# Kernel tuning notes

Measured on AMD Instinct MI355X. Metric: run time of the kernel, lower is better.

Reference implementation:

```python
import jax, jax.numpy as jnp
import numpy as np

N_NODES = 50000
IN_CH = 128
HID = 128
OUT_CH = 64
N_EDGES = 800000


def _glorot(key, shape):
    fan_in, fan_out = shape[1], shape[0]
    lim = (6.0 / (fan_in + fan_out)) ** 0.5
    return jax.random.uniform(key, shape, jnp.float32, -lim, lim)


def setup_inputs() -> dict:
    key = jax.random.key(0)
    ks = jax.random.split(key, 10)
    x = jax.random.normal(ks[0], (N_NODES, IN_CH), jnp.float32)
    edge_index = jax.random.randint(ks[1], (2, N_EDGES), 0, N_NODES, jnp.int64)
    return {
        "x": x,
        "edge_index": edge_index,
        # SAGEConv 1: in -> hidden (lin_l has bias, lin_r no bias)
        "Wl1": _glorot(ks[2], (HID, IN_CH)),
        "bl1": jnp.zeros((HID,), jnp.float32),
        "Wr1": _glorot(ks[3], (HID, IN_CH)),
        # SAGEConv 2: hidden -> hidden
        "Wl2": _glorot(ks[4], (HID, HID)),
        "bl2": jnp.zeros((HID,), jnp.float32),
        "Wr2": _glorot(ks[5], (HID, HID)),
        # final Linear hidden -> out
        "Wout": _glorot(ks[6], (OUT_CH, HID)),
        "bout": jnp.zeros((OUT_CH,), jnp.float32),
    }


def _sage_conv(x, src, dst, Wl, bl, Wr, n_nodes):
    # mean-aggregate neighbor features: scatter x[src] into dst buckets
    msg = x[src]                                              # [E, C]
    agg = jax.ops.segment_sum(msg, dst, num_segments=n_nodes)  # [N, C]
    cnt = jax.ops.segment_sum(jnp.ones((src.shape[0],), x.dtype), dst,
                              num_segments=n_nodes)            # [N]
    agg = agg / jnp.maximum(cnt, 1.0)[:, None]
    return agg @ Wl.T + bl + x @ Wr.T


def reference(x, edge_index, Wl1, bl1, Wr1, Wl2, bl2, Wr2, Wout, bout):
    src, dst = edge_index[0], edge_index[1]
    n = x.shape[0]
    h = _sage_conv(x, src, dst, Wl1, bl1, Wr1, n)
    h = jax.nn.relu(h)
    h = _sage_conv(h, src, dst, Wl2, bl2, Wr2, n)
    logits = h @ Wout.T + bout
    return jax.nn.log_softmax(logits, axis=1)
```

## Files before the change

### kernel.cpp

```cpp
#include <hip/hip_runtime.h>

#define N_NODES 50000
#define N_EDGES 800000
#define HID 128
#define OUT_CH 64
#define LDA 264
#define BSHIFT 6
#define NBUCKET ((N_NODES + 63) >> BSHIFT)
#define NCHUNK 256
#define CHUNK_E (N_EDGES / NCHUNK)
#define BCAP 2560

typedef __attribute__((ext_vector_type(8))) short bf16x8;
typedef __attribute__((ext_vector_type(4))) float f32x4;

__device__ __forceinline__ float bf2f(unsigned int bits16) {
    return __uint_as_float(bits16 << 16);
}
__device__ __forceinline__ unsigned short f2bf(float f) {
    unsigned int u = __float_as_uint(f);
    u = (u + 0x7fffu + ((u >> 16) & 1u)) >> 16;
    return (unsigned short)u;
}
__device__ __forceinline__ void acc_u4(float* a, uint4 v) {
    a[0] += bf2f(v.x & 0xffffu); a[1] += bf2f(v.x >> 16);
    a[2] += bf2f(v.y & 0xffffu); a[3] += bf2f(v.y >> 16);
    a[4] += bf2f(v.z & 0xffffu); a[5] += bf2f(v.z >> 16);
    a[6] += bf2f(v.w & 0xffffu); a[7] += bf2f(v.w >> 16);
}

__global__ __launch_bounds__(256) void convert_x_kernel(
    const float* __restrict__ x, unsigned short* __restrict__ xb)
{
    int gid = blockIdx.x * 256 + threadIdx.x;
    int node = gid >> 5, c4 = gid & 31;
    float4 v = reinterpret_cast<const float4*>(x + (size_t)node * HID)[c4];
    unsigned short* o = xb + (size_t)node * HID + c4 * 4;
    o[0] = f2bf(v.x); o[1] = f2bf(v.y); o[2] = f2bf(v.z); o[3] = f2bf(v.w);
}

__global__ __launch_bounds__(256) void swizzle_w_kernel(
    const float* __restrict__ Wl1, const float* __restrict__ Wr1,
    const float* __restrict__ Wl2, const float* __restrict__ Wr2,
    const float* __restrict__ Wout,
    unsigned short* __restrict__ w1s, unsigned short* __restrict__ w2s,
    unsigned short* __restrict__ wos)
{
    int fid = blockIdx.x * 256 + threadIdx.x;
    if (fid < 8192) {
        int layer = fid >> 12;
        int r = fid & 4095;
        int lane = r & 63, ks = (r >> 6) & 7, t = r >> 9;
        int col = t * 16 + (lane & 15);
        int kb = ks * 32 + (lane >> 4) * 8;
        const float* Wl = layer ? Wl2 : Wl1;
        const float* Wr = layer ? Wr2 : Wr1;
        unsigned short* o = (layer ? w2s : w1s) + (size_t)r * 8;
        #pragma unroll
        for (int j = 0; j < 8; ++j) {
            int k = kb + j;
            float v = (k < 128) ? Wl[(size_t)col * 128 + k] : Wr[(size_t)col * 128 + (k - 128)];
            o[j] = f2bf(v);
        }
    } else if (fid < 9216) {
        int r = fid - 8192;
        int lane = r & 63, ks = (r >> 6) & 3, t = r >> 8;
        int col = t * 16 + (lane & 15);
        int kb = ks * 32 + (lane >> 4) * 8;
        unsigned short* o = wos + (size_t)r * 8;
        #pragma unroll
        for (int j = 0; j < 8; ++j)
            o[j] = f2bf(Wout[(size_t)col * 128 + kb + j]);
    }
}

__global__ __launch_bounds__(256) void histb_kernel(const int* __restrict__ dst,
                                                    int* __restrict__ histg) {
    __shared__ int h[NBUCKET];
    for (int i = threadIdx.x; i < NBUCKET; i += 256) h[i] = 0;
    __syncthreads();
    const int e0 = blockIdx.x * CHUNK_E;
    for (int i = threadIdx.x; i < CHUNK_E; i += 256)
        atomicAdd(&h[dst[e0 + i] >> BSHIFT], 1);
    __syncthreads();
    for (int i = threadIdx.x; i < NBUCKET; i += 256)
        histg[i * NCHUNK + blockIdx.x] = h[i];
}

__global__ __launch_bounds__(256) void scanA2_kernel(const int* __restrict__ histg,
                                                     int* __restrict__ partial) {
    const int tid = threadIdx.x;
    int v = histg[blockIdx.x * 256 + tid];
    const int lane = tid & 63, wave = tid >> 6;
    int incl = v;
    #pragma unroll
    for (int off = 1; off < 64; off <<= 1) {
        int t = __shfl_up(incl, off);
        if (lane >= off) incl += t;
    }
    __shared__ int wsum[4];
    if (lane == 63) wsum[wave] = incl;
    __syncthreads();
    if (tid == 0) partial[blockIdx.x] = wsum[0] + wsum[1] + wsum[2] + wsum[3];
}

__global__ __launch_bounds__(256) void scanB2_kernel(int* __restrict__ partial) {
    const int tid = threadIdx.x;
    int vals[4]; int sum = 0;
    #pragma unroll
    for (int j = 0; j < 4; ++j) {
        int idx = tid * 4 + j;
        vals[j] = (idx < NBUCKET) ? partial[idx] : 0;
        sum += vals[j];
    }
    const int lane = tid & 63, wave = tid >> 6;
    int incl = sum;
    #pragma unroll
    for (int off = 1; off < 64; off <<= 1) {
        int t = __shfl_up(incl, off);
        if (lane >= off) incl += t;
    }
    __shared__ int wsum[4];
    if (lane == 63) wsum[wave] = incl;
    __syncthreads();
    int base = 0;
    if (wave > 0) base += wsum[0];
    if (wave > 1) base += wsum[1];
    if (wave > 2) base += wsum[2];
    int run = base + incl - sum;
    #pragma unroll
    for (int j = 0; j < 4; ++j) {
        int idx = tid * 4 + j;
        if (idx < NBUCKET) { int c = vals[j]; partial[idx] = run; run += c; }
    }
}

__global__ __launch_bounds__(256) void scanC2_kernel(int* __restrict__ histg,
                                                     const int* __restrict__ partial) {
    const int tid = threadIdx.x;
    const int i = blockIdx.x * 256 + tid;
    int v = histg[i];
    const int lane = tid & 63, wave = tid >> 6;
    int incl = v;
    #pragma unroll
    for (int off = 1; off < 64; off <<= 1) {
        int t = __shfl_up(incl, off);
        if (lane >= off) incl += t;
    }
    __shared__ int wsum[4];
    if (lane == 63) wsum[wave] = incl;
    __syncthreads();
    int base = partial[blockIdx.x];
    if (wave > 0) base += wsum[0];
    if (wave > 1) base += wsum[1];
    if (wave > 2) base += wsum[2];
    histg[i] = base + incl - v;
}

__global__ __launch_bounds__(256) void binA_kernel(
    const int* __restrict__ src, const int* __restrict__ dst,
    const int* __restrict__ obase, unsigned* __restrict__ epack)
{
    __shared__ int cur[NBUCKET];
    for (int i = threadIdx.x; i < NBUCKET; i += 256)
        cur[i] = obase[i * NCHUNK + blockIdx.x];
    __syncthreads();
    const int e0 = blockIdx.x * CHUNK_E;
    for (int i = threadIdx.x; i < CHUNK_E; i += 256) {
        int d = dst[e0 + i];
        int p = atomicAdd(&cur[d >> BSHIFT], 1);
        epack[p] = (unsigned)src[e0 + i] | ((unsigned)(d & 63) << 16);
    }
}

__global__ __launch_bounds__(256) void bucket_sort_kernel(
    const unsigned* __restrict__ epack, const int* __restrict__ obase,
    int* __restrict__ row_ptr, unsigned short* __restrict__ esrc)
{
    __shared__ unsigned lpack[BCAP];
    __shared__ unsigned short lout[BCAP];
    __shared__ int deg[64], cur[64];
    const int b = blockIdx.x;
    const int tid = threadIdx.x;
    const int regBeg = obase[b * NCHUNK];
    const int regEnd = (b + 1 < NBUCKET) ? obase[(b + 1) * NCHUNK] : N_EDGES;
    const int cnt = regEnd - regBeg;

    if (tid < 64) deg[tid] = 0;
    __syncthreads();
    for (int i = tid; i < cnt; i += 256) {
        unsigned p = epack[regBeg + i];
        if (i < BCAP) lpack[i] = p;
        atomicAdd(&deg[(p >> 16) & 63], 1);
    }
    __syncthreads();
    if (tid < 64) {
        int v = deg[tid];
        int incl = v;
        #pragma unroll
        for (int off = 1; off < 64; off <<= 1) {
            int t = __shfl_up(incl, off);
            if (tid >= off) incl += t;
        }
        int pre = incl - v;
        cur[tid] = pre;
        int node = b * 64 + tid;
        if (node < N_NODES) row_ptr[node] = regBeg + pre;
    }
    if (b == NBUCKET - 1 && tid == 0) row_ptr[N_NODES] = N_EDGES;
    __syncthreads();
    for (int i = tid; i < cnt; i += 256) {
        unsigned p = (i < BCAP) ? lpack[i] : epack[regBeg + i];
        int q = atomicAdd(&cur[(p >> 16) & 63], 1);
        unsigned short s = (unsigned short)(p & 0xffffu);
        if (q < BCAP) lout[q] = s;
        else esrc[regBeg + q] = s;
    }
    __syncthreads();
    const int lim = (cnt < BCAP) ? cnt : BCAP;
    for (int i = tid; i < lim; i += 256)
        esrc[regBeg + i] = lout[i];
}

__global__ __launch_bounds__(256) void gather_kernel(
    const unsigned short* __restrict__ feat,
    const int* __restrict__ row_ptr, const unsigned short* __restrict__ esrc,
    unsigned short* __restrict__ agg)
{
    const int tid = threadIdx.x;
    const int wave = tid >> 6, lane = tid & 63;
    const int g = lane >> 4, c = lane & 15;
    const int gw0 = blockIdx.x * 4 + wave;
    const int NW = gridDim.x * 4;
    const int NGROUP = N_NODES / 4;

    for (int grp = gw0; grp < NGROUP; grp += NW) {
        const int base = grp * 4;
        int beg[4], deg[4], ids[4];
        int rp0 = row_ptr[base];
        #pragma unroll
        for (int j = 0; j < 4; ++j) {
            int rp1 = row_ptr[base + j + 1];
            beg[j] = rp0; deg[j] = rp1 - rp0; rp0 = rp1;
        }
        #pragma unroll
        for (int j = 0; j < 4; ++j) {
            int idx = beg[j] + c;
            idx = (idx < N_EDGES) ? idx : (N_EDGES - 1);
            ids[j] = esrc[idx];
        }

        float acc[4][8];
        #pragma unroll
        for (int j = 0; j < 4; ++j)
            #pragma unroll
            for (int k = 0; k < 8; ++k) acc[j][k] = 0.0f;

        #pragma unroll
        for (int jp = 0; jp < 2; ++jp) {
            uint4 v[2][4];
            #pragma unroll
            for (int jj = 0; jj < 2; ++jj) {
                const int j = jp * 2 + jj;
                #pragma unroll
                for (int b = 0; b < 4; ++b) {
                    int s = __shfl(ids[j], b * 4 + g);
                    v[jj][b] = *reinterpret_cast<const uint4*>(feat + (size_t)s * HID + c * 8);
                }
            }
            #pragma unroll
            for (int jj = 0; jj < 2; ++jj) {
                const int j = jp * 2 + jj;
                #pragma unroll
                for (int b = 0; b < 4; ++b) {
                    uint4 vv = v[jj][b];
                    if (b * 4 + g >= deg[j]) vv = make_uint4(0u, 0u, 0u, 0u);
                    acc_u4(acc[j], vv);
                }
            }
            #pragma unroll
            for (int jj = 0; jj < 2; ++jj) {
                const int j = jp * 2 + jj;
                const int last = beg[j] + deg[j] - 1;
                for (int e0 = 16; e0 < deg[j]; e0 += 16) {
                    int idx = beg[j] + e0 + c;
                    int id2 = esrc[(idx < last) ? idx : last];
                    uint4 w[4];
                    #pragma unroll
                    for (int b = 0; b < 4; ++b) {
                        int s = __shfl(id2, b * 4 + g);
                        w[b] = *reinterpret_cast<const uint4*>(feat + (size_t)s * HID + c * 8);
                    }
                    #pragma unroll
                    for (int b = 0; b < 4; ++b) {
                        uint4 vv = w[b];
                        if (e0 + b * 4 + g >= deg[j]) vv = make_uint4(0u, 0u, 0u, 0u);
                        acc_u4(acc[j], vv);
                    }
                }
            }
        }

        #pragma unroll
        for (int j = 0; j < 4; ++j) {
            const float scale = 1.0f / fmaxf((float)deg[j], 1.0f);
            float r[8];
            #pragma unroll
            for (int k = 0; k < 8; ++k) {
                float t = acc[j][k];
                t += __shfl_xor(t, 16);
                t += __shfl_xor(t, 32);
                r[k] = t * scale;
            }
            if (g == 0) {
                uint4 pk;
                pk.x = (unsigned)f2bf(r[0]) | ((unsigned)f2bf(r[1]) << 16);
                pk.y = (unsigned)f2bf(r[2]) | ((unsigned)f2bf(r[3]) << 16);
                pk.z = (unsigned)f2bf(r[4]) | ((unsigned)f2bf(r[5]) << 16);
                pk.w = (unsigned)f2bf(r[6]) | ((unsigned)f2bf(r[7]) << 16);
                *reinterpret_cast<uint4*>(agg + (size_t)(base + j) * HID + c * 8) = pk;
            }
        }
    }
}

__global__ __launch_bounds__(256) void sage_gemm_kernel(
    const unsigned short* __restrict__ aggIn,
    const unsigned short* __restrict__ selfIn,
    const unsigned short* __restrict__ wsz,
    const float* __restrict__ bias,
    unsigned short* __restrict__ Hout, int relu)
{
    __shared__ unsigned short sA[16 * LDA];
    const int tid = threadIdx.x;
    const int wave = tid >> 6, lane = tid & 63;
    const int m0 = blockIdx.x * 16;

    {
        int r = tid >> 4, cc = tid & 15;
        *reinterpret_cast<uint4*>(&sA[r * LDA + cc * 8]) =
            reinterpret_cast<const uint4*>(aggIn + (size_t)(m0 + r) * HID)[cc];
        *reinterpret_cast<uint4*>(&sA[r * LDA + 128 + cc * 8]) =
            reinterpret_cast<const uint4*>(selfIn + (size_t)(m0 + r) * HID)[cc];
    }
    __syncthreads();

    const int l15 = lane & 15, lq = lane >> 4;
    bf16x8 bfrag[2][8];
    #pragma unroll
    for (int nt = 0; nt < 2; ++nt) {
        const unsigned short* wb = wsz + ((size_t)(wave * 2 + nt) * 8) * 64 * 8 + lane * 8;
        #pragma unroll
        for (int ks = 0; ks < 8; ++ks)
            bfrag[nt][ks] = *reinterpret_cast<const bf16x8*>(wb + (size_t)ks * 64 * 8);
    }
    f32x4 acc0 = {0.f, 0.f, 0.f, 0.f}, acc1 = {0.f, 0.f, 0.f, 0.f};
    #pragma unroll
    for (int ks = 0; ks < 8; ++ks) {
        bf16x8 af = *reinterpret_cast<const bf16x8*>(&sA[l15 * LDA + ks * 32 + lq * 8]);
        acc0 = __builtin_amdgcn_mfma_f32_16x16x32_bf16(af, bfrag[0][ks], acc0, 0, 0, 0);
        acc1 = __builtin_amdgcn_mfma_f32_16x16x32_bf16(af, bfrag[1][ks], acc1, 0, 0, 0);
    }
    const int n0 = wave * 32;
    #pragma unroll
    for (int nt = 0; nt < 2; ++nt) {
        const f32x4 a = nt ? acc1 : acc0;
        const int col = n0 + nt * 16 + l15;
        const float bv = bias[col];
        #pragma unroll
        for (int r = 0; r < 4; ++r) {
            float v = a[r] + bv;
            if (relu) v = fmaxf(v, 0.0f);
            Hout[(size_t)(m0 + lq * 4 + r) * HID + col] = f2bf(v);
        }
    }
}

__global__ __launch_bounds__(256) void final_gemm_kernel(
    const unsigned short* __restrict__ aggIn,
    const unsigned short* __restrict__ selfIn,
    const unsigned short* __restrict__ wsz2,
    const float* __restrict__ bl2,
    const unsigned short* __restrict__ wos,
    const float* __restrict__ bout,
    float* __restrict__ out)
{
    __shared__ unsigned short sA[16 * LDA];
    __shared__ float sL[16][OUT_CH];
    const int tid = threadIdx.x;
    const int wave = tid >> 6, lane = tid & 63;
    const int m0 = blockIdx.x * 16;

    {
        int r = tid >> 4, cc = tid & 15;
        *reinterpret_cast<uint4*>(&sA[r * LDA + cc * 8]) =
            reinterpret_cast<const uint4*>(aggIn + (size_t)(m0 + r) * HID)[cc];
        *reinterpret_cast<uint4*>(&sA[r * LDA + 128 + cc * 8]) =
            reinterpret_cast<const uint4*>(selfIn + (size_t)(m0 + r) * HID)[cc];
    }
    __syncthreads();

    const int l15 = lane & 15, lq = lane >> 4;
    bf16x8 bfrag[2][8];
    #pragma unroll
    for (int nt = 0; nt < 2; ++nt) {
        const unsigned short* wb = wsz2 + ((size_t)(wave * 2 + nt) * 8) * 64 * 8 + lane * 8;
        #pragma unroll
        for (int ks = 0; ks < 8; ++ks)
            bfrag[nt][ks] = *reinterpret_cast<const bf16x8*>(wb + (size_t)ks * 64 * 8);
    }
    f32x4 acc0 = {0.f, 0.f, 0.f, 0.f}, acc1 = {0.f, 0.f, 0.f, 0.f};
    #pragma unroll
    for (int ks = 0; ks < 8; ++ks) {
        bf16x8 af = *reinterpret_cast<const bf16x8*>(&sA[l15 * LDA + ks * 32 + lq * 8]);
        acc0 = __builtin_amdgcn_mfma_f32_16x16x32_bf16(af, bfrag[0][ks], acc0, 0, 0, 0);
        acc1 = __builtin_amdgcn_mfma_f32_16x16x32_bf16(af, bfrag[1][ks], acc1, 0, 0, 0);
    }
    __syncthreads();

    const int n0 = wave * 32;
    #pragma unroll
    for (int nt = 0; nt < 2; ++nt) {
        const f32x4 a = nt ? acc1 : acc0;
        const int col = n0 + nt * 16 + l15;
        const float bv = bl2[col];
        #pragma unroll
        for (int r = 0; r < 4; ++r)
            sA[(lq * 4 + r) * LDA + col] = f2bf(a[r] + bv);
    }
    __syncthreads();

    {
        f32x4 hacc = {0.f, 0.f, 0.f, 0.f};
        #pragma unroll
        for (int ks = 0; ks < 4; ++ks) {
            bf16x8 af = *reinterpret_cast<const bf16x8*>(&sA[l15 * LDA + ks * 32 + lq * 8]);
            bf16x8 bf = *reinterpret_cast<const bf16x8*>(
                wos + ((size_t)(wave * 4 + ks)) * 64 * 8 + lane * 8);
            hacc = __builtin_amdgcn_mfma_f32_16x16x32_bf16(af, bf, hacc, 0, 0, 0);
        }
        const int col = wave * 16 + l15;
        const float bo = bout[col];
        #pragma unroll
        for (int r = 0; r < 4; ++r)
            sL[lq * 4 + r][col] = hacc[r] + bo;
    }
    __syncthreads();

    for (int r = wave; r < 16; r += 4) {
        float v = sL[r][lane];
        float m = v;
        for (int off = 32; off; off >>= 1) m = fmaxf(m, __shfl_xor(m, off));
        float ex = expf(v - m);
        float s = ex;
        for (int off = 32; off; off >>= 1) s += __shfl_xor(s, off);
        out[(size_t)(m0 + r) * OUT_CH + lane] = v - m - logf(s);
    }
}

extern "C" void kernel_launch(void* const* d_in, const int* in_sizes, int n_in,
                              void* d_out, int out_size, void* d_ws, size_t ws_size,
                              hipStream_t stream) {
    const float* x    = (const float*)d_in[0];
    const int*   edge = (const int*)d_in[1];
    const int*   src  = edge;
    const int*   dst  = edge + N_EDGES;
    const float* Wl1  = (const float*)d_in[2];
    const float* bl1  = (const float*)d_in[3];
    const float* Wr1  = (const float*)d_in[4];
    const float* Wl2  = (const float*)d_in[5];
    const float* bl2  = (const float*)d_in[6];
    const float* Wr2  = (const float*)d_in[7];
    const float* Wout = (const float*)d_in[8];
    const float* bout = (const float*)d_in[9];
    float* out = (float*)d_out;

    char* ws = (char*)d_ws;
    const size_t featBytes = (size_t)N_NODES * HID * 2;
    unsigned short* xb  = (unsigned short*)ws;
    unsigned short* h1  = (unsigned short*)(ws + featBytes);
    unsigned short* agg = (unsigned short*)(ws + 2 * featBytes);
    char* p = ws + 3 * featBytes;
    int* row_ptr = (int*)p;          p += (size_t)(N_NODES + 1) * 4 + 252;
    int* histg   = (int*)p;          p += (size_t)NBUCKET * NCHUNK * 4;
    int* partial = (int*)p;          p += (size_t)NBUCKET * 4 + 72;
    unsigned* epack = (unsigned*)p;  p += (size_t)N_EDGES * 4;
    unsigned short* esrc = (unsigned short*)p;  p += (size_t)N_EDGES * 2;
    unsigned short* w1s = (unsigned short*)p;   p += 128 * 256 * 2;
    unsigned short* w2s = (unsigned short*)p;   p += 128 * 256 * 2;
    unsigned short* wos = (unsigned short*)p;

    convert_x_kernel<<<N_NODES * 32 / 256, 256, 0, stream>>>(x, xb);
    swizzle_w_kernel<<<36, 256, 0, stream>>>(Wl1, Wr1, Wl2, Wr2, Wout, w1s, w2s, wos);
    histb_kernel<<<NCHUNK, 256, 0, stream>>>(dst, histg);
    scanA2_kernel<<<NBUCKET, 256, 0, stream>>>(histg, partial);
    scanB2_kernel<<<1, 256, 0, stream>>>(partial);
    scanC2_kernel<<<NBUCKET, 256, 0, stream>>>(histg, partial);
    binA_kernel<<<NCHUNK, 256, 0, stream>>>(src, dst, histg, epack);
    bucket_sort_kernel<<<NBUCKET, 256, 0, stream>>>(epack, histg, row_ptr, esrc);

    gather_kernel<<<2048, 256, 0, stream>>>(xb, row_ptr, esrc, agg);
    sage_gemm_kernel<<<N_NODES / 16, 256, 0, stream>>>(agg, xb, w1s, bl1, h1, 1);
    gather_kernel<<<2048, 256, 0, stream>>>(h1, row_ptr, esrc, agg);
    final_gemm_kernel<<<N_NODES / 16, 256, 0, stream>>>(agg, h1, w2s, bl2,
                                                        wos, bout, out);
}
```

Measured before the change: 133.1 us.

## Gather layer-1 neighbor features from an FP8 copy of x and merge prep kernels

```diff
diff --git a/kernel.cpp b/kernel.cpp
--- a/kernel.cpp
+++ b/kernel.cpp
@@ -10,6 +10,7 @@
 #define NCHUNK 256
 #define CHUNK_E (N_EDGES / NCHUNK)
 #define BCAP 2560
+#define GATHER_BLOCKS 1563
 
 typedef __attribute__((ext_vector_type(8))) short bf16x8;
 typedef __attribute__((ext_vector_type(4))) float f32x4;
@@ -29,48 +30,83 @@
     a[6] += bf2f(v.w & 0xffffu); a[7] += bf2f(v.w >> 16);
 }
 
-__global__ __launch_bounds__(256) void convert_x_kernel(
-    const float* __restrict__ x, unsigned short* __restrict__ xb)
-{
-    int gid = blockIdx.x * 256 + threadIdx.x;
-    int node = gid >> 5, c4 = gid & 31;
-    float4 v = reinterpret_cast<const float4*>(x + (size_t)node * HID)[c4];
-    unsigned short* o = xb + (size_t)node * HID + c4 * 4;
-    o[0] = f2bf(v.x); o[1] = f2bf(v.y); o[2] = f2bf(v.z); o[3] = f2bf(v.w);
-}
-
-__global__ __launch_bounds__(256) void swizzle_w_kernel(
+__device__ __forceinline__ unsigned int f2fp8(float f) {
+    unsigned int u = __float_as_uint(f);
+    unsigned int s = (u >> 24) & 0x80u;
+    float xa = fabsf(f);
+    if (xa >= 0.015625f) {
+        unsigned int a = __float_as_uint(xa);
+        if (a > 0x43E00000u) a = 0x43E00000u;
+        unsigned int r = a + 0x0007FFFFu + ((a >> 20) & 1u);
+        unsigned int e8 = r >> 23;
+        if (e8 > 135u) { r = 0x43E00000u; e8 = 135u; }
+        return s | (((e8 - 120u) << 3) | ((r >> 20) & 7u));
+    } else {
+        int q = (int)(xa * 512.0f + 0.5f);
+        return s | (unsigned int)q;
+    }
+}
+__device__ __forceinline__ void acc_fp8x4(float* a, unsigned int u) {
+#if __has_builtin(__builtin_amdgcn_cvt_pk_f32_fp8)
+    auto p0 = __builtin_amdgcn_cvt_pk_f32_fp8(u, false);
+    auto p1 = __builtin_amdgcn_cvt_pk_f32_fp8(u, true);
+    a[0] += p0[0]; a[1] += p0[1]; a[2] += p1[0]; a[3] += p1[1];
+#else
+    #pragma unroll
+    for (int i = 0; i < 4; ++i) {
+        unsigned int b = (u >> (8 * i)) & 0xffu;
+        float d = __uint_as_float(((b & 0x7fu) << 20) | ((b & 0x80u) << 24));
+        a[i] = fmaf(d, 0x1p120f, a[i]);
+    }
+#endif
+}
+
+__global__ __launch_bounds__(256) void prep_kernel(
+    const float* __restrict__ x, unsigned short* __restrict__ xb,
+    unsigned char* __restrict__ x8,
     const float* __restrict__ Wl1, const float* __restrict__ Wr1,
     const float* __restrict__ Wl2, const float* __restrict__ Wr2,
     const float* __restrict__ Wout,
     unsigned short* __restrict__ w1s, unsigned short* __restrict__ w2s,
     unsigned short* __restrict__ wos)
 {
-    int fid = blockIdx.x * 256 + threadIdx.x;
-    if (fid < 8192) {
-        int layer = fid >> 12;
-        int r = fid & 4095;
-        int lane = r & 63, ks = (r >> 6) & 7, t = r >> 9;
-        int col = t * 16 + (lane & 15);
-        int kb = ks * 32 + (lane >> 4) * 8;
-        const float* Wl = layer ? Wl2 : Wl1;
-        const float* Wr = layer ? Wr2 : Wr1;
-        unsigned short* o = (layer ? w2s : w1s) + (size_t)r * 8;
-        #pragma unroll
-        for (int j = 0; j < 8; ++j) {
-            int k = kb + j;
-            float v = (k < 128) ? Wl[(size_t)col * 128 + k] : Wr[(size_t)col * 128 + (k - 128)];
-            o[j] = f2bf(v);
-        }
-    } else if (fid < 9216) {
-        int r = fid - 8192;
-        int lane = r & 63, ks = (r >> 6) & 3, t = r >> 8;
-        int col = t * 16 + (lane & 15);
-        int kb = ks * 32 + (lane >> 4) * 8;
-        unsigned short* o = wos + (size_t)r * 8;
-        #pragma unroll
-        for (int j = 0; j < 8; ++j)
-            o[j] = f2bf(Wout[(size_t)col * 128 + kb + j]);
+    const int XB = N_NODES * 32 / 256;
+    const int b = blockIdx.x;
+    if (b < XB) {
+        int gid = b * 256 + threadIdx.x;
+        int node = gid >> 5, c4 = gid & 31;
+        float4 v = reinterpret_cast<const float4*>(x + (size_t)node * HID)[c4];
+        unsigned short* o = xb + (size_t)node * HID + c4 * 4;
+        o[0] = f2bf(v.x); o[1] = f2bf(v.y); o[2] = f2bf(v.z); o[3] = f2bf(v.w);
+        unsigned int pk8 = f2fp8(v.x) | (f2fp8(v.y) << 8) | (f2fp8(v.z) << 16) | (f2fp8(v.w) << 24);
+        *reinterpret_cast<unsigned int*>(x8 + (size_t)node * HID + c4 * 4) = pk8;
+    } else {
+        int fid = (b - XB) * 256 + threadIdx.x;
+        if (fid < 8192) {
+            int layer = fid >> 12;
+            int r = fid & 4095;
+            int lane = r & 63, ks = (r >> 6) & 7, t = r >> 9;
+            int col = t * 16 + (lane & 15);
+            int kb = ks * 32 + (lane >> 4) * 8;
+            const float* Wl = layer ? Wl2 : Wl1;
+            const float* Wr = layer ? Wr2 : Wr1;
+            unsigned short* o = (layer ? w2s : w1s) + (size_t)r * 8;
+            #pragma unroll
+            for (int j = 0; j < 8; ++j) {
+                int k = kb + j;
+                float v = (k < 128) ? Wl[(size_t)col * 128 + k] : Wr[(size_t)col * 128 + (k - 128)];
+                o[j] = f2bf(v);
+            }
+        } else if (fid < 9216) {
+            int r = fid - 8192;
+            int lane = r & 63, ks = (r >> 6) & 3, t = r >> 8;
+            int col = t * 16 + (lane & 15);
+            int kb = ks * 32 + (lane >> 4) * 8;
+            unsigned short* o = wos + (size_t)r * 8;
+            #pragma unroll
+            for (int j = 0; j < 8; ++j)
+                o[j] = f2bf(Wout[(size_t)col * 128 + kb + j]);
+        }
     }
 }
 
@@ -324,6 +360,110 @@
     }
 }
 
+__global__ __launch_bounds__(256) void gather_fp8_kernel(
+    const unsigned char* __restrict__ feat8,
+    const int* __restrict__ row_ptr, const unsigned short* __restrict__ esrc,
+    unsigned short* __restrict__ agg)
+{
+    const int tid = threadIdx.x;
+    const int wave = tid >> 6, lane = tid & 63;
+    const int g = lane >> 4, c = lane & 15;
+    const int gw0 = blockIdx.x * 4 + wave;
+    const int NW = gridDim.x * 4;
+    const int NGROUP = N_NODES / 4;
+
+    for (int grp = gw0; grp < NGROUP; grp += NW) {
+        const int base = grp * 4;
+        int beg[4], deg[4], ids[4];
+        int rp0 = row_ptr[base];
+        #pragma unroll
+        for (int j = 0; j < 4; ++j) {
+            int rp1 = row_ptr[base + j + 1];
+            beg[j] = rp0; deg[j] = rp1 - rp0; rp0 = rp1;
+        }
+        #pragma unroll
+        for (int j = 0; j < 4; ++j) {
+            int idx = beg[j] + c;
+            idx = (idx < N_EDGES) ? idx : (N_EDGES - 1);
+            ids[j] = esrc[idx];
+        }
+
+        float acc[4][8];
+        #pragma unroll
+        for (int j = 0; j < 4; ++j)
+            #pragma unroll
+            for (int k = 0; k < 8; ++k) acc[j][k] = 0.0f;
+
+        #pragma unroll
+        for (int jp = 0; jp < 2; ++jp) {
+            uint2 v[2][4];
+            #pragma unroll
+            for (int jj = 0; jj < 2; ++jj) {
+                const int j = jp * 2 + jj;
+                #pragma unroll
+                for (int b = 0; b < 4; ++b) {
+                    int s = __shfl(ids[j], b * 4 + g);
+                    v[jj][b] = *reinterpret_cast<const uint2*>(feat8 + (size_t)s * HID + c * 8);
+                }
+            }
+            #pragma unroll
+            for (int jj = 0; jj < 2; ++jj) {
+                const int j = jp * 2 + jj;
+                #pragma unroll
+                for (int b = 0; b < 4; ++b) {
+                    uint2 vv = v[jj][b];
+                    if (b * 4 + g >= deg[j]) vv = make_uint2(0u, 0u);
+                    acc_fp8x4(&acc[j][0], vv.x);
+                    acc_fp8x4(&acc[j][4], vv.y);
+                }
+            }
+            #pragma unroll
+            for (int jj = 0; jj < 2; ++jj) {
+                const int j = jp * 2 + jj;
+                const int last = beg[j] + deg[j] - 1;
+                for (int e0 = 16; e0 < deg[j]; e0 += 16) {
+                    int idx = beg[j] + e0 + c;
+                    int id2 = esrc[(idx < last) ? idx : last];
+                    uint2 w[4];
+                    #pragma unroll
+                    for (int b = 0; b < 4; ++b) {
+                        int s = __shfl(id2, b * 4 + g);
+                        w[b] = *reinterpret_cast<const uint2*>(feat8 + (size_t)s * HID + c * 8);
+                    }
+                    #pragma unroll
+                    for (int b = 0; b < 4; ++b) {
+                        uint2 vv = w[b];
+                        if (e0 + b * 4 + g >= deg[j]) vv = make_uint2(0u, 0u);
+                        acc_fp8x4(&acc[j][0], vv.x);
+                        acc_fp8x4(&acc[j][4], vv.y);
+                    }
+                }
+            }
+        }
+
+        #pragma unroll
+        for (int j = 0; j < 4; ++j) {
+            const float scale = 1.0f / fmaxf((float)deg[j], 1.0f);
+            float r[8];
+            #pragma unroll
+            for (int k = 0; k < 8; ++k) {
+                float t = acc[j][k];
+                t += __shfl_xor(t, 16);
+                t += __shfl_xor(t, 32);
+                r[k] = t * scale;
+            }
+            if (g == 0) {
+                uint4 pk;
+                pk.x = (unsigned)f2bf(r[0]) | ((unsigned)f2bf(r[1]) << 16);
+                pk.y = (unsigned)f2bf(r[2]) | ((unsigned)f2bf(r[3]) << 16);
+                pk.z = (unsigned)f2bf(r[4]) | ((unsigned)f2bf(r[5]) << 16);
+                pk.w = (unsigned)f2bf(r[6]) | ((unsigned)f2bf(r[7]) << 16);
+                *reinterpret_cast<uint4*>(agg + (size_t)(base + j) * HID + c * 8) = pk;
+            }
+        }
+    }
+}
+
 __global__ __launch_bounds__(256) void sage_gemm_kernel(
     const unsigned short* __restrict__ aggIn,
     const unsigned short* __restrict__ selfIn,
@@ -476,11 +616,13 @@
     float* out = (float*)d_out;
 
     char* ws = (char*)d_ws;
-    const size_t featBytes = (size_t)N_NODES * HID * 2;
+    const size_t featBytes  = (size_t)N_NODES * HID * 2;
+    const size_t feat8Bytes = (size_t)N_NODES * HID;
     unsigned short* xb  = (unsigned short*)ws;
     unsigned short* h1  = (unsigned short*)(ws + featBytes);
     unsigned short* agg = (unsigned short*)(ws + 2 * featBytes);
-    char* p = ws + 3 * featBytes;
+    unsigned char*  x8  = (unsigned char*)(ws + 3 * featBytes);
+    char* p = ws + 3 * featBytes + feat8Bytes;
     int* row_ptr = (int*)p;          p += (size_t)(N_NODES + 1) * 4 + 252;
     int* histg   = (int*)p;          p += (size_t)NBUCKET * NCHUNK * 4;
     int* partial = (int*)p;          p += (size_t)NBUCKET * 4 + 72;
@@ -490,8 +632,8 @@
     unsigned short* w2s = (unsigned short*)p;   p += 128 * 256 * 2;
     unsigned short* wos = (unsigned short*)p;
 
-    convert_x_kernel<<<N_NODES * 32 / 256, 256, 0, stream>>>(x, xb);
-    swizzle_w_kernel<<<36, 256, 0, stream>>>(Wl1, Wr1, Wl2, Wr2, Wout, w1s, w2s, wos);
+    prep_kernel<<<N_NODES * 32 / 256 + 36, 256, 0, stream>>>(
+        x, xb, x8, Wl1, Wr1, Wl2, Wr2, Wout, w1s, w2s, wos);
     histb_kernel<<<NCHUNK, 256, 0, stream>>>(dst, histg);
     scanA2_kernel<<<NBUCKET, 256, 0, stream>>>(histg, partial);
     scanB2_kernel<<<1, 256, 0, stream>>>(partial);
@@ -499,9 +641,9 @@
     binA_kernel<<<NCHUNK, 256, 0, stream>>>(src, dst, histg, epack);
     bucket_sort_kernel<<<NBUCKET, 256, 0, stream>>>(epack, histg, row_ptr, esrc);
 
-    gather_kernel<<<2048, 256, 0, stream>>>(xb, row_ptr, esrc, agg);
+    gather_fp8_kernel<<<GATHER_BLOCKS, 256, 0, stream>>>(x8, row_ptr, esrc, agg);
     sage_gemm_kernel<<<N_NODES / 16, 256, 0, stream>>>(agg, xb, w1s, bl1, h1, 1);
-    gather_kernel<<<2048, 256, 0, stream>>>(h1, row_ptr, esrc, agg);
+    gather_kernel<<<GATHER_BLOCKS, 256, 0, stream>>>(h1, row_ptr, esrc, agg);
     final_gemm_kernel<<<N_NODES / 16, 256, 0, stream>>>(agg, h1, w2s, bl2,
                                                         wos, bout, out);
 }
```

New measurement: 131.9 us. About the same (-0.9%).
